# Performance work log

Measured on AMD Instinct MI355X. Metric: run time of the kernel, lower is better.

The kernel has to match this reference:

```python
import jax, jax.numpy as jnp
import numpy as np

HIDDEN = 1024
NUM_HEADS = 16
HEAD_DIM = HIDDEN // NUM_HEADS  # 64
B, LQ, LK = 2, 2048, 2048


def setup_inputs() -> dict:
    key = jax.random.key(0)
    ks = jax.random.split(key, 9)
    s = 1.0 / np.sqrt(HIDDEN)
    return {
        "hidden_states_query": jax.random.normal(ks[0], (B, LQ, HIDDEN), jnp.float32),
        "hidden_states_key": jax.random.normal(ks[1], (B, LK, HIDDEN), jnp.float32),
        "attention_mask": jnp.ones((B, LQ, LK), jnp.float32),
        "Wq": jax.random.normal(ks[2], (HIDDEN, HIDDEN), jnp.float32) * s,
        "bq": jax.random.normal(ks[3], (HIDDEN,), jnp.float32) * s,
        "Wk": jax.random.normal(ks[4], (HIDDEN, HIDDEN), jnp.float32) * s,
        "bk": jax.random.normal(ks[5], (HIDDEN,), jnp.float32) * s,
        "Wv": jax.random.normal(ks[6], (HIDDEN, HIDDEN), jnp.float32) * s,
        "bv": jax.random.normal(ks[7], (HIDDEN,), jnp.float32) * s,
    }


def _split_heads(x):
    # [B, L, H*D] -> [B, nH, L, D]
    b, l, _ = x.shape
    return x.reshape(b, l, NUM_HEADS, HEAD_DIM).transpose(0, 2, 1, 3)


def reference(hidden_states_query, hidden_states_key, attention_mask, Wq, bq, Wk, bk, Wv, bv):
    # nn.Linear applies x @ W.T + b; weights here stored as [out, in]
    q = _split_heads(hidden_states_query @ Wq.T + bq)
    k = _split_heads(hidden_states_key @ Wk.T + bk)
    v = _split_heads(hidden_states_key @ Wv.T + bv)
    scale = 1.0 / np.sqrt(HEAD_DIM)
    scores = jnp.einsum("bhqd,bhkd->bhqk", q * scale, k)  # [B, nH, Lq, Lk]
    # mask: 1 -> 0, 0 -> -10000, broadcast over heads
    scores = scores + ((1.0 - attention_mask) * -10000.0)[:, None, :, :]
    probs = jax.nn.softmax(scores, axis=-1)
    ctx = jnp.einsum("bhqk,bhkd->bhqd", probs, v)
    b, h, lq, d = ctx.shape
    return ctx.transpose(0, 2, 1, 3).reshape(b, lq, h * d)
```

## Files before the change

### kernel.cpp

```cpp
#include <hip/hip_runtime.h>
#include <hip/hip_bf16.h>

#define HID 1024
#define NH 16
#define HD 64
#define SEQ 2048
#define NB 2
#define NTOK (NB * SEQ)

typedef __attribute__((ext_vector_type(8))) short bf16x8;
typedef __attribute__((ext_vector_type(4))) float f32x4;

#define QSCALE 0.18033688011112042f
#define MASKSCALE 1.4426950408889634f

__device__ __forceinline__ unsigned short f2bf(float f) {
    unsigned u = __builtin_bit_cast(unsigned, f);
    u += 0x7FFFu + ((u >> 16) & 1u);
    return (unsigned short)(u >> 16);
}
__device__ __forceinline__ unsigned cvtpk(float a, float b) {
    unsigned r;
    asm("v_cvt_pk_bf16_f32 %0, %1, %2" : "=v"(r) : "v"(a), "v"(b));
    return r;
}
__device__ __forceinline__ void gload_lds16(const unsigned short* g, unsigned short* l) {
    __builtin_amdgcn_global_load_lds(
        (const __attribute__((address_space(1))) unsigned int*)g,
        (__attribute__((address_space(3))) unsigned int*)l, 16, 0, 0);
}

__global__ __launch_bounds__(256) void cvt_all(
    const float* __restrict__ xq, const float* __restrict__ xk,
    const float* __restrict__ Wq, const float* __restrict__ Wk, const float* __restrict__ Wv,
    const float* __restrict__ mask,
    unsigned short* __restrict__ dxq, unsigned short* __restrict__ dxk,
    unsigned short* __restrict__ dwq, unsigned short* __restrict__ dwk,
    unsigned short* __restrict__ dwv, int* __restrict__ flags) {
    const int id = blockIdx.x;
    if (id >= 11264) {
        const int lane = threadIdx.x & 63;
        int i = ((id - 11264) * 256 + threadIdx.x) * 4;
        float4 v = *(const float4*)(mask + i);
        bool ok = (v.x == 1.0f) && (v.y == 1.0f) && (v.z == 1.0f) && (v.w == 1.0f);
        unsigned long long bal = __ballot(ok);
        int g = lane >> 4;
        if ((lane & 15) == 0) {
            unsigned m16 = (unsigned)(bal >> (g * 16)) & 0xFFFFu;
            if (m16 != 0xFFFFu) {
                int b = i >> 22;
                int rem = i & 4194303;
                int q = rem >> 11, k = rem & 2047;
                atomicAnd(&flags[(b << 10) + ((q >> 6) << 5) + (k >> 6)], 0);
            }
        }
        return;
    }
    const float* src;
    unsigned short* dst;
    int base;
    float scale = 1.0f;
    if (id < 4096)       { src = xq; dst = dxq; base = 0; }
    else if (id < 8192)  { src = xk; dst = dxk; base = 4096; }
    else if (id < 9216)  { src = Wq; dst = dwq; base = 8192; scale = QSCALE; }
    else if (id < 10240) { src = Wk; dst = dwk; base = 9216; }
    else                 { src = Wv; dst = dwv; base = 10240; }
    int i = ((id - base) * 256 + threadIdx.x) * 4;
    float4 v = *(const float4*)(src + i);
    ushort4 o;
    o.x = f2bf(v.x * scale); o.y = f2bf(v.y * scale);
    o.z = f2bf(v.z * scale); o.w = f2bf(v.w * scale);
    *(ushort4*)(dst + i) = o;
}

__global__ __launch_bounds__(256) void proj_gemm(
    const unsigned short* __restrict__ xq, const unsigned short* __restrict__ xk,
    const unsigned short* __restrict__ wq, const unsigned short* __restrict__ wk,
    const unsigned short* __restrict__ wv,
    const float* __restrict__ bq, const float* __restrict__ bk, const float* __restrict__ bv,
    unsigned short* __restrict__ Qh, unsigned short* __restrict__ Kh,
    unsigned short* __restrict__ Vt) {
    __shared__ __align__(16) unsigned short As[128 * 32];
    __shared__ __align__(16) unsigned short Bs[128 * 32];

    const int z = blockIdx.z;
    const unsigned short *A, *B;
    const float* bias;
    float bsc;
    unsigned short* out;
    int mt, nt;
    bool tr;
    if (z == 0)      { A = xq; B = wq; bias = bq; bsc = QSCALE; out = Qh; tr = false; mt = blockIdx.x; nt = blockIdx.y; }
    else if (z == 1) { A = xk; B = wk; bias = bk; bsc = 1.0f;  out = Kh; tr = false; mt = blockIdx.x; nt = blockIdx.y; }
    else             { A = wv; B = xk; bias = bv; bsc = 1.0f;  out = Vt; tr = true;
                       mt = blockIdx.x & 7; nt = blockIdx.y * 4 + (blockIdx.x >> 3); }
    const int m0 = mt * 128, n0 = nt * 128;
    const int tid = threadIdx.x, wave = tid >> 6, lane = tid & 63;
    const int wr = (wave >> 1) * 64, wc = (wave & 1) * 64;
    const int frow = lane & 15, fk = (lane >> 4) * 8;
    const int srow = lane >> 2, skb = (lane & 3) * 8;

    f32x4 acc[4][4] = {};

    for (int k0 = 0; k0 < HID; k0 += 32) {
        __syncthreads();
#pragma unroll
        for (int t = 0; t < 2; ++t) {
            int c = t * 4 + wave;
            gload_lds16(A + (size_t)(m0 + c * 16 + srow) * HID + k0 + skb, &As[c * 512]);
            gload_lds16(B + (size_t)(n0 + c * 16 + srow) * HID + k0 + skb, &Bs[c * 512]);
        }
        __syncthreads();
        bf16x8 af[4], bfr[4];
#pragma unroll
        for (int i = 0; i < 4; ++i) af[i] = *(const bf16x8*)&As[(wr + i * 16 + frow) * 32 + fk];
#pragma unroll
        for (int j = 0; j < 4; ++j) bfr[j] = *(const bf16x8*)&Bs[(wc + j * 16 + frow) * 32 + fk];
#pragma unroll
        for (int i = 0; i < 4; ++i)
#pragma unroll
            for (int j = 0; j < 4; ++j)
                acc[i][j] = __builtin_amdgcn_mfma_f32_16x16x32_bf16(af[i], bfr[j], acc[i][j], 0, 0, 0);
    }

#pragma unroll
    for (int i = 0; i < 4; ++i)
#pragma unroll
        for (int j = 0; j < 4; ++j)
#pragma unroll
            for (int r = 0; r < 4; ++r) {
                int row = m0 + wr + i * 16 + (lane >> 4) * 4 + r;
                int col = n0 + wc + j * 16 + frow;
                float v = acc[i][j][r];
                if (!tr) {
                    v += bsc * bias[col];
                    int b = row >> 11, l = row & 2047, hh = col >> 6, d = col & 63;
                    out[(((size_t)(b * NH + hh)) * SEQ + l) * HD + d] = f2bf(v);
                } else {
                    v += bias[row];
                    int b = col >> 11, l = col & 2047, hh = row >> 6, d = row & 63;
                    out[(((size_t)(b * NH + hh)) * HD + d) * SEQ + l] = f2bf(v);
                }
            }
}

__global__ __launch_bounds__(256) void flash_attn(
    const unsigned short* __restrict__ Qh, const unsigned short* __restrict__ Kh,
    const unsigned short* __restrict__ Vt, const float* __restrict__ mask,
    const int* __restrict__ flags, float* __restrict__ out) {
    __shared__ __align__(16) unsigned short Ks[2][64 * 64];
    __shared__ __align__(16) unsigned short Vs[2][64 * 64];
    __shared__ __align__(16) unsigned short Ps[4][16 * 64];

    const int tid = threadIdx.x, wave = tid >> 6, lane = tid & 63;
    const int id = blockIdx.x;
    const int bh = (id & 7) * 4 + ((id >> 3) & 3);
    const int qi = id >> 5;
    const int b = bh >> 4, h = bh & 15;
    const size_t hoff = (size_t)bh * SEQ * HD;
    const int fr = lane & 15, hi = lane >> 4;
    const int f7 = fr & 7, swz3 = f7 << 3;
    const int qa = qi * 64 + wave * 16 + fr;

    bf16x8 qfa0 = *(const bf16x8*)&Qh[hoff + (size_t)qa * HD + hi * 8];
    bf16x8 qfa1 = *(const bf16x8*)&Qh[hoff + (size_t)qa * HD + 32 + hi * 8];

    const float* mrowA = mask + (size_t)b * SEQ * SEQ + (size_t)qa * SEQ;
    const int* frow = flags + (b << 10) + (qi << 5);
    int fv = frow[lane & 31];
    const unsigned long long bm = __ballot(fv != 0);

    const int srow = wave * 8 + (lane >> 3);
    const int sch = (lane & 7) ^ (srow & 7);
    const unsigned short* kbase = Kh + hoff + (size_t)srow * HD + (sch << 3);
    const unsigned short* vbase = Vt + hoff + (size_t)srow * SEQ + (sch << 3);

    f32x4 accA[4] = {};
    f32x4 laccA = {};
    const bf16x8 ones = {0x3F80, 0x3F80, 0x3F80, 0x3F80, 0x3F80, 0x3F80, 0x3F80, 0x3F80};

#define STAGE(bi, t)                                                              \
    do {                                                                          \
        gload_lds16(kbase + (size_t)(t) * 64 * HD, &Ks[bi][(wave * 8) * 64]);     \
        gload_lds16(kbase + (size_t)((t) * 64 + 32) * HD,                         \
                    &Ks[bi][(wave * 8 + 32) * 64]);                               \
        gload_lds16(vbase + (t) * 64, &Vs[bi][(wave * 8) * 64]);                  \
        gload_lds16(vbase + (size_t)32 * SEQ + (t) * 64,                          \
                    &Vs[bi][(wave * 8 + 32) * 64]);                               \
    } while (0)

    STAGE(0, 0);
    __syncthreads();
    int buf = 0;

    for (int t = 0; t < 32; ++t) {
        if (t < 31) STAGE(buf ^ 1, t + 1);
        const unsigned short* ks = Ks[buf];
        const unsigned short* vs = Vs[buf];

        f32x4 sA[4];
        __builtin_amdgcn_s_setprio(1);
#pragma unroll
        for (int sub = 0; sub < 4; ++sub) {
            const int rbase = (sub * 16 + fr) * 64;
            bf16x8 kf0 = *(const bf16x8*)&ks[rbase + ((hi << 3) ^ swz3)];
            bf16x8 kf1 = *(const bf16x8*)&ks[rbase + (((hi + 4) << 3) ^ swz3)];
            f32x4 z = {0.f, 0.f, 0.f, 0.f};
            z = __builtin_amdgcn_mfma_f32_16x16x32_bf16(kf0, qfa0, z, 0, 0, 0);
            z = __builtin_amdgcn_mfma_f32_16x16x32_bf16(kf1, qfa1, z, 0, 0, 0);
            sA[sub] = z;
        }
        __builtin_amdgcn_s_setprio(0);

        if (!((bm >> t) & 1)) {
            const int k0 = t * 64;
#pragma unroll
            for (int sub = 0; sub < 4; ++sub) {
                float4 ma = *(const float4*)&mrowA[k0 + sub * 16 + hi * 4];
                sA[sub][0] += (1.f - ma.x) * (-10000.f * MASKSCALE);
                sA[sub][1] += (1.f - ma.y) * (-10000.f * MASKSCALE);
                sA[sub][2] += (1.f - ma.z) * (-10000.f * MASKSCALE);
                sA[sub][3] += (1.f - ma.w) * (-10000.f * MASKSCALE);
            }
        }

#pragma unroll
        for (int sub = 0; sub < 4; ++sub)
#pragma unroll
            for (int r = 0; r < 4; ++r)
                sA[sub][r] = __builtin_amdgcn_exp2f(sA[sub][r]);

#pragma unroll
        for (int sub = 0; sub < 4; ++sub) {
            const int uoff = ((((sub << 1) + (hi >> 1)) ^ f7) << 3) + ((hi & 1) << 2);
            uint2 ua = {cvtpk(sA[sub][0], sA[sub][1]), cvtpk(sA[sub][2], sA[sub][3])};
            *(uint2*)&Ps[wave][fr * 64 + uoff] = ua;
        }

        bf16x8 pA0 = *(const bf16x8*)&Ps[wave][fr * 64 + ((hi ^ f7) << 3)];
        bf16x8 pA1 = *(const bf16x8*)&Ps[wave][fr * 64 + (((hi + 4) ^ f7) << 3)];

        __builtin_amdgcn_s_setprio(1);
        laccA = __builtin_amdgcn_mfma_f32_16x16x32_bf16(ones, pA0, laccA, 0, 0, 0);
        laccA = __builtin_amdgcn_mfma_f32_16x16x32_bf16(ones, pA1, laccA, 0, 0, 0);

#pragma unroll
        for (int sub = 0; sub < 4; ++sub) {
            const int rbase = (sub * 16 + fr) * 64;
            bf16x8 vf0 = *(const bf16x8*)&vs[rbase + ((hi << 3) ^ swz3)];
            bf16x8 vf1 = *(const bf16x8*)&vs[rbase + (((hi + 4) << 3) ^ swz3)];
            accA[sub] = __builtin_amdgcn_mfma_f32_16x16x32_bf16(vf0, pA0, accA[sub], 0, 0, 0);
            accA[sub] = __builtin_amdgcn_mfma_f32_16x16x32_bf16(vf1, pA1, accA[sub], 0, 0, 0);
        }
        __builtin_amdgcn_s_setprio(0);

        if (t < 31) {
            __syncthreads();
            buf ^= 1;
        }
    }

    float rA = 1.0f / laccA[0];
#pragma unroll
    for (int sub = 0; sub < 4; ++sub) {
        float4 oA = {accA[sub][0] * rA, accA[sub][1] * rA, accA[sub][2] * rA, accA[sub][3] * rA};
        *(float4*)&out[((size_t)b * SEQ + qa) * HID + h * HD + sub * 16 + hi * 4] = oA;
    }
#undef STAGE
}

extern "C" void kernel_launch(void* const* d_in, const int* in_sizes, int n_in,
                              void* d_out, int out_size, void* d_ws, size_t ws_size,
                              hipStream_t stream) {
    const float* xq = (const float*)d_in[0];
    const float* xk = (const float*)d_in[1];
    const float* mask = (const float*)d_in[2];
    const float* Wq = (const float*)d_in[3];
    const float* bq = (const float*)d_in[4];
    const float* Wk = (const float*)d_in[5];
    const float* bk = (const float*)d_in[6];
    const float* Wv = (const float*)d_in[7];
    const float* bv = (const float*)d_in[8];
    float* out = (float*)d_out;

    const size_t NX = (size_t)NTOK * HID;
    const size_t NW = (size_t)HID * HID;
    const size_t need = (5 * NX + 3 * NW) * sizeof(unsigned short) + 2048 * sizeof(int);
    if (ws_size < need) return;

    unsigned short* ws = (unsigned short*)d_ws;
    unsigned short* xq_b = ws;
    unsigned short* xk_b = xq_b + NX;
    unsigned short* wq_b = xk_b + NX;
    unsigned short* wk_b = wq_b + NW;
    unsigned short* wv_b = wk_b + NW;
    unsigned short* Qh = wv_b + NW;
    unsigned short* Kh = Qh + NX;
    unsigned short* Vt = Kh + NX;
    int* flags = (int*)(Vt + NX);

    hipMemsetAsync(flags, 0xFF, 2048 * sizeof(int), stream);
    cvt_all<<<19456, 256, 0, stream>>>(xq, xk, Wq, Wk, Wv, mask,
                                       xq_b, xk_b, wq_b, wk_b, wv_b, flags);
    proj_gemm<<<dim3(32, 8, 3), 256, 0, stream>>>(xq_b, xk_b, wq_b, wk_b, wv_b,
                                                  bq, bk, bv, Qh, Kh, Vt);
    flash_attn<<<1024, 256, 0, stream>>>(Qh, Kh, Vt, mask, flags, out);
}
```

Baseline: 121.8 us.

## Double-buffer projection GEMM loads and keep P fragments in registers via permuted V layout

The projection GEMM now double-buffers its LDS tiles: it prefetches the next K-slice while computing the current one and needs one barrier per iteration instead of two. The attention kernel drops the per-wave LDS round trip for the probability matrix. It packs the exp results directly into MFMA B-operand registers, and V^T columns are stored with a permuted sequence index so the register layout matches the reduction order. This removes LDS writes and reads plus latency in the inner attention loop, at the cost of doubled GEMM LDS use and a layout coupling that must match the K ordering exactly.

```diff
diff --git a/kernel.cpp b/kernel.cpp
--- a/kernel.cpp
+++ b/kernel.cpp
@@ -10,6 +10,7 @@
 
 typedef __attribute__((ext_vector_type(8))) short bf16x8;
 typedef __attribute__((ext_vector_type(4))) float f32x4;
+typedef __attribute__((ext_vector_type(4))) unsigned u32x4;
 
 #define QSCALE 0.18033688011112042f
 #define MASKSCALE 1.4426950408889634f
@@ -80,8 +81,8 @@
     const float* __restrict__ bq, const float* __restrict__ bk, const float* __restrict__ bv,
     unsigned short* __restrict__ Qh, unsigned short* __restrict__ Kh,
     unsigned short* __restrict__ Vt) {
-    __shared__ __align__(16) unsigned short As[128 * 32];
-    __shared__ __align__(16) unsigned short Bs[128 * 32];
+    __shared__ __align__(16) unsigned short As[2][128 * 32];
+    __shared__ __align__(16) unsigned short Bs[2][128 * 32];
 
     const int z = blockIdx.z;
     const unsigned short *A, *B;
@@ -100,27 +101,41 @@
     const int frow = lane & 15, fk = (lane >> 4) * 8;
     const int srow = lane >> 2, skb = (lane & 3) * 8;
 
+    const unsigned short* Ab = A + (size_t)(m0 + wave * 16 + srow) * HID + skb;
+    const unsigned short* Bb = B + (size_t)(n0 + wave * 16 + srow) * HID + skb;
+
     f32x4 acc[4][4] = {};
 
-    for (int k0 = 0; k0 < HID; k0 += 32) {
-        __syncthreads();
-#pragma unroll
-        for (int t = 0; t < 2; ++t) {
-            int c = t * 4 + wave;
-            gload_lds16(A + (size_t)(m0 + c * 16 + srow) * HID + k0 + skb, &As[c * 512]);
-            gload_lds16(B + (size_t)(n0 + c * 16 + srow) * HID + k0 + skb, &Bs[c * 512]);
-        }
-        __syncthreads();
+#define PSTAGE(bi, k0)                                                                 \
+    do {                                                                               \
+        gload_lds16(Ab + (k0), &As[bi][wave * 512]);                                   \
+        gload_lds16(Ab + (size_t)64 * HID + (k0), &As[bi][2048 + wave * 512]);         \
+        gload_lds16(Bb + (k0), &Bs[bi][wave * 512]);                                   \
+        gload_lds16(Bb + (size_t)64 * HID + (k0), &Bs[bi][2048 + wave * 512]);         \
+    } while (0)
+
+    PSTAGE(0, 0);
+    __syncthreads();
+    int buf = 0;
+
+    for (int it = 0; it < 32; ++it) {
+        if (it < 31) PSTAGE(buf ^ 1, (it + 1) * 32);
         bf16x8 af[4], bfr[4];
 #pragma unroll
-        for (int i = 0; i < 4; ++i) af[i] = *(const bf16x8*)&As[(wr + i * 16 + frow) * 32 + fk];
-#pragma unroll
-        for (int j = 0; j < 4; ++j) bfr[j] = *(const bf16x8*)&Bs[(wc + j * 16 + frow) * 32 + fk];
+        for (int i = 0; i < 4; ++i) af[i] = *(const bf16x8*)&As[buf][(wr + i * 16 + frow) * 32 + fk];
+#pragma unroll
+        for (int j = 0; j < 4; ++j) bfr[j] = *(const bf16x8*)&Bs[buf][(wc + j * 16 + frow) * 32 + fk];
+        __builtin_amdgcn_s_setprio(1);
 #pragma unroll
         for (int i = 0; i < 4; ++i)
 #pragma unroll
             for (int j = 0; j < 4; ++j)
                 acc[i][j] = __builtin_amdgcn_mfma_f32_16x16x32_bf16(af[i], bfr[j], acc[i][j], 0, 0, 0);
+        __builtin_amdgcn_s_setprio(0);
+        if (it < 31) {
+            __syncthreads();
+            buf ^= 1;
+        }
     }
 
 #pragma unroll
@@ -138,10 +153,12 @@
                     out[(((size_t)(b * NH + hh)) * SEQ + l) * HD + d] = f2bf(v);
                 } else {
                     v += bias[row];
-                    int b = col >> 11, l = col & 2047, hh = row >> 6, d = row & 63;
-                    out[(((size_t)(b * NH + hh)) * HD + d) * SEQ + l] = f2bf(v);
+                    int b = col >> 11, ll = col & 2047, hh = row >> 6, d = row & 63;
+                    int lp = (ll & ~0x1C) | ((ll & 0x0C) << 1) | ((ll & 0x10) >> 2);
+                    out[(((size_t)(b * NH + hh)) * HD + d) * SEQ + lp] = f2bf(v);
                 }
             }
+#undef PSTAGE
 }
 
 __global__ __launch_bounds__(256) void flash_attn(
@@ -150,7 +167,6 @@
     const int* __restrict__ flags, float* __restrict__ out) {
     __shared__ __align__(16) unsigned short Ks[2][64 * 64];
     __shared__ __align__(16) unsigned short Vs[2][64 * 64];
-    __shared__ __align__(16) unsigned short Ps[4][16 * 64];
 
     const int tid = threadIdx.x, wave = tid >> 6, lane = tid & 63;
     const int id = blockIdx.x;
@@ -230,15 +246,13 @@
             for (int r = 0; r < 4; ++r)
                 sA[sub][r] = __builtin_amdgcn_exp2f(sA[sub][r]);
 
-#pragma unroll
-        for (int sub = 0; sub < 4; ++sub) {
-            const int uoff = ((((sub << 1) + (hi >> 1)) ^ f7) << 3) + ((hi & 1) << 2);
-            uint2 ua = {cvtpk(sA[sub][0], sA[sub][1]), cvtpk(sA[sub][2], sA[sub][3])};
-            *(uint2*)&Ps[wave][fr * 64 + uoff] = ua;
-        }
-
-        bf16x8 pA0 = *(const bf16x8*)&Ps[wave][fr * 64 + ((hi ^ f7) << 3)];
-        bf16x8 pA1 = *(const bf16x8*)&Ps[wave][fr * 64 + (((hi + 4) ^ f7) << 3)];
+        u32x4 w0, w1;
+        w0[0] = cvtpk(sA[0][0], sA[0][1]); w0[1] = cvtpk(sA[0][2], sA[0][3]);
+        w0[2] = cvtpk(sA[1][0], sA[1][1]); w0[3] = cvtpk(sA[1][2], sA[1][3]);
+        w1[0] = cvtpk(sA[2][0], sA[2][1]); w1[1] = cvtpk(sA[2][2], sA[2][3]);
+        w1[2] = cvtpk(sA[3][0], sA[3][1]); w1[3] = cvtpk(sA[3][2], sA[3][3]);
+        bf16x8 pA0 = __builtin_bit_cast(bf16x8, w0);
+        bf16x8 pA1 = __builtin_bit_cast(bf16x8, w1);
 
         __builtin_amdgcn_s_setprio(1);
         laccA = __builtin_amdgcn_mfma_f32_16x16x32_bf16(ones, pA0, laccA, 0, 0, 0);
```

New measurement: 120.5 us. Within noise of the previous version (-1.1%).

## Triple-buffer projection GEMM with 256x128 tiles and keep P in registers

Applied to the files above, without the earlier changes.

The projection GEMM moves to 512-thread blocks with 256x128 tiles, a three-stage LDS ring with explicit vmcnt waits and a single barrier per k-step, and an XOR swizzle on the LDS layout. This is meant to overlap global loads with MFMA work and cut barrier and bank-conflict stalls. In flash attention, the P matrix is packed straight into MFMA operands instead of taking an LDS round trip, which is made correct by permuting the sequence index when V^T is written. The attention loop is also unrolled by two with fixed buffer pointers. The risks are lower GEMM occupancy from the larger LDS footprint and subtle layout coupling between the two kernels.

```diff
diff --git a/kernel.cpp b/kernel.cpp
--- a/kernel.cpp
+++ b/kernel.cpp
@@ -10,9 +10,12 @@
 
 typedef __attribute__((ext_vector_type(8))) short bf16x8;
 typedef __attribute__((ext_vector_type(4))) float f32x4;
+typedef __attribute__((ext_vector_type(4))) unsigned u32x4;
 
 #define QSCALE 0.18033688011112042f
 #define MASKSCALE 1.4426950408889634f
+
+#define MFMA16(a, b, c) __builtin_amdgcn_mfma_f32_16x16x32_bf16((a), (b), (c), 0, 0, 0)
 
 __device__ __forceinline__ unsigned short f2bf(float f) {
     unsigned u = __builtin_bit_cast(unsigned, f);
@@ -73,15 +76,15 @@
     *(ushort4*)(dst + i) = o;
 }
 
-__global__ __launch_bounds__(256) void proj_gemm(
+__global__ __launch_bounds__(512, 4) void proj_gemm(
     const unsigned short* __restrict__ xq, const unsigned short* __restrict__ xk,
     const unsigned short* __restrict__ wq, const unsigned short* __restrict__ wk,
     const unsigned short* __restrict__ wv,
     const float* __restrict__ bq, const float* __restrict__ bk, const float* __restrict__ bv,
     unsigned short* __restrict__ Qh, unsigned short* __restrict__ Kh,
     unsigned short* __restrict__ Vt) {
-    __shared__ __align__(16) unsigned short As[128 * 32];
-    __shared__ __align__(16) unsigned short Bs[128 * 32];
+    __shared__ __align__(16) unsigned short As[3][256 * 32];
+    __shared__ __align__(16) unsigned short Bs[3][128 * 32];
 
     const int z = blockIdx.z;
     const unsigned short *A, *B;
@@ -90,56 +93,87 @@
     unsigned short* out;
     int mt, nt;
     bool tr;
-    if (z == 0)      { A = xq; B = wq; bias = bq; bsc = QSCALE; out = Qh; tr = false; mt = blockIdx.x; nt = blockIdx.y; }
-    else if (z == 1) { A = xk; B = wk; bias = bk; bsc = 1.0f;  out = Kh; tr = false; mt = blockIdx.x; nt = blockIdx.y; }
+    if (z == 0)      { A = xq; B = wq; bias = bq; bsc = QSCALE; out = Qh; tr = false;
+                       mt = blockIdx.x & 15; nt = blockIdx.x >> 4; }
+    else if (z == 1) { A = xk; B = wk; bias = bk; bsc = 1.0f;  out = Kh; tr = false;
+                       mt = blockIdx.x & 15; nt = blockIdx.x >> 4; }
     else             { A = wv; B = xk; bias = bv; bsc = 1.0f;  out = Vt; tr = true;
-                       mt = blockIdx.x & 7; nt = blockIdx.y * 4 + (blockIdx.x >> 3); }
-    const int m0 = mt * 128, n0 = nt * 128;
+                       mt = blockIdx.x & 3; nt = blockIdx.x >> 2; }
+    const int m0 = mt * 256, n0 = nt * 128;
     const int tid = threadIdx.x, wave = tid >> 6, lane = tid & 63;
-    const int wr = (wave >> 1) * 64, wc = (wave & 1) * 64;
-    const int frow = lane & 15, fk = (lane >> 4) * 8;
-    const int srow = lane >> 2, skb = (lane & 3) * 8;
-
-    f32x4 acc[4][4] = {};
-
-    for (int k0 = 0; k0 < HID; k0 += 32) {
-        __syncthreads();
-#pragma unroll
-        for (int t = 0; t < 2; ++t) {
-            int c = t * 4 + wave;
-            gload_lds16(A + (size_t)(m0 + c * 16 + srow) * HID + k0 + skb, &As[c * 512]);
-            gload_lds16(B + (size_t)(n0 + c * 16 + srow) * HID + k0 + skb, &Bs[c * 512]);
+    const int wm = wave >> 2, wn = wave & 3;
+    const int fr = lane & 15, hi = lane >> 4;
+    const int fswz = (hi ^ ((fr >> 1) & 3)) << 3;
+
+    const int arow = wave * 16 + (lane >> 2);
+    const int aunit = (lane & 3) ^ ((lane >> 3) & 3);
+    const unsigned short* Asrc = A + (size_t)(m0 + arow) * HID + aunit * 8;
+    const unsigned short* Bsrc = B + (size_t)(n0 + arow) * HID + aunit * 8;
+
+    unsigned short *a0 = As[0], *a1 = As[1], *a2 = As[2];
+    unsigned short *b0 = Bs[0], *b1 = Bs[1], *b2 = Bs[2];
+
+    f32x4 acc[8][2] = {};
+
+#define PSTG(ap, bp, k0)                                                         \
+    do {                                                                         \
+        gload_lds16(Asrc + (k0), (ap) + wave * 512);                             \
+        gload_lds16(Asrc + (size_t)128 * HID + (k0), (ap) + 4096 + wave * 512);  \
+        gload_lds16(Bsrc + (k0), (bp) + wave * 512);                             \
+    } while (0)
+
+    PSTG(a0, b0, 0);
+    PSTG(a1, b1, 32);
+
+    for (int t = 0; t < 32; ++t) {
+        if (t < 31) asm volatile("s_waitcnt vmcnt(3)" ::: "memory");
+        else        asm volatile("s_waitcnt vmcnt(0)" ::: "memory");
+        __builtin_amdgcn_s_barrier();
+
+        bf16x8 bfr0 = *(const bf16x8*)&b0[(wn * 32 + fr) * 32 + fswz];
+        bf16x8 bfr1 = *(const bf16x8*)&b0[(wn * 32 + 16 + fr) * 32 + fswz];
+        if (t < 30) {
+            gload_lds16(Asrc + (t + 2) * 32, a2 + wave * 512);
+            gload_lds16(Asrc + (size_t)128 * HID + (t + 2) * 32, a2 + 4096 + wave * 512);
         }
-        __syncthreads();
-        bf16x8 af[4], bfr[4];
-#pragma unroll
-        for (int i = 0; i < 4; ++i) af[i] = *(const bf16x8*)&As[(wr + i * 16 + frow) * 32 + fk];
-#pragma unroll
-        for (int j = 0; j < 4; ++j) bfr[j] = *(const bf16x8*)&Bs[(wc + j * 16 + frow) * 32 + fk];
-#pragma unroll
-        for (int i = 0; i < 4; ++i)
-#pragma unroll
-            for (int j = 0; j < 4; ++j)
-                acc[i][j] = __builtin_amdgcn_mfma_f32_16x16x32_bf16(af[i], bfr[j], acc[i][j], 0, 0, 0);
+#pragma unroll
+        for (int mh = 0; mh < 2; ++mh) {
+            bf16x8 af[4];
+#pragma unroll
+            for (int i = 0; i < 4; ++i)
+                af[i] = *(const bf16x8*)&a0[(wm * 128 + mh * 64 + i * 16 + fr) * 32 + fswz];
+            if (mh == 0 && t < 30) gload_lds16(Bsrc + (t + 2) * 32, b2 + wave * 512);
+            __builtin_amdgcn_s_setprio(1);
+#pragma unroll
+            for (int i = 0; i < 4; ++i) {
+                acc[mh * 4 + i][0] = MFMA16(af[i], bfr0, acc[mh * 4 + i][0]);
+                acc[mh * 4 + i][1] = MFMA16(af[i], bfr1, acc[mh * 4 + i][1]);
+            }
+            __builtin_amdgcn_s_setprio(0);
+        }
+        unsigned short* ta = a0; a0 = a1; a1 = a2; a2 = ta;
+        unsigned short* tb = b0; b0 = b1; b1 = b2; b2 = tb;
     }
-
-#pragma unroll
-    for (int i = 0; i < 4; ++i)
-#pragma unroll
-        for (int j = 0; j < 4; ++j)
+#undef PSTG
+
+#pragma unroll
+    for (int ii = 0; ii < 8; ++ii)
+#pragma unroll
+        for (int j = 0; j < 2; ++j)
 #pragma unroll
             for (int r = 0; r < 4; ++r) {
-                int row = m0 + wr + i * 16 + (lane >> 4) * 4 + r;
-                int col = n0 + wc + j * 16 + frow;
-                float v = acc[i][j][r];
+                int row = m0 + wm * 128 + ii * 16 + hi * 4 + r;
+                int col = n0 + wn * 32 + j * 16 + fr;
+                float v = acc[ii][j][r];
                 if (!tr) {
                     v += bsc * bias[col];
                     int b = row >> 11, l = row & 2047, hh = col >> 6, d = col & 63;
                     out[(((size_t)(b * NH + hh)) * SEQ + l) * HD + d] = f2bf(v);
                 } else {
                     v += bias[row];
-                    int b = col >> 11, l = col & 2047, hh = row >> 6, d = row & 63;
-                    out[(((size_t)(b * NH + hh)) * HD + d) * SEQ + l] = f2bf(v);
+                    int b = col >> 11, ll = col & 2047, hh = row >> 6, d = row & 63;
+                    int lp = (ll & ~0x1C) | ((ll & 0x0C) << 1) | ((ll & 0x10) >> 2);
+                    out[(((size_t)(b * NH + hh)) * HD + d) * SEQ + lp] = f2bf(v);
                 }
             }
 }
@@ -150,7 +184,6 @@
     const int* __restrict__ flags, float* __restrict__ out) {
     __shared__ __align__(16) unsigned short Ks[2][64 * 64];
     __shared__ __align__(16) unsigned short Vs[2][64 * 64];
-    __shared__ __align__(16) unsigned short Ps[4][16 * 64];
 
     const int tid = threadIdx.x, wave = tid >> 6, lane = tid & 63;
     const int id = blockIdx.x;
@@ -172,93 +205,92 @@
 
     const int srow = wave * 8 + (lane >> 3);
     const int sch = (lane & 7) ^ (srow & 7);
-    const unsigned short* kbase = Kh + hoff + (size_t)srow * HD + (sch << 3);
-    const unsigned short* vbase = Vt + hoff + (size_t)srow * SEQ + (sch << 3);
+    const unsigned short* kp = Kh + hoff + (size_t)srow * HD + (sch << 3);
+    const unsigned short* vp = Vt + hoff + (size_t)srow * SEQ + (sch << 3);
 
     f32x4 accA[4] = {};
     f32x4 laccA = {};
     const bf16x8 ones = {0x3F80, 0x3F80, 0x3F80, 0x3F80, 0x3F80, 0x3F80, 0x3F80, 0x3F80};
 
-#define STAGE(bi, t)                                                              \
-    do {                                                                          \
-        gload_lds16(kbase + (size_t)(t) * 64 * HD, &Ks[bi][(wave * 8) * 64]);     \
-        gload_lds16(kbase + (size_t)((t) * 64 + 32) * HD,                         \
-                    &Ks[bi][(wave * 8 + 32) * 64]);                               \
-        gload_lds16(vbase + (t) * 64, &Vs[bi][(wave * 8) * 64]);                  \
-        gload_lds16(vbase + (size_t)32 * SEQ + (t) * 64,                          \
-                    &Vs[bi][(wave * 8 + 32) * 64]);                               \
+    unsigned short* const ks0 = &Ks[0][0];
+    unsigned short* const ks1 = &Ks[1][0];
+    unsigned short* const vs0 = &Vs[0][0];
+    unsigned short* const vs1 = &Vs[1][0];
+
+#define STG(ksd, vsd)                                                            \
+    do {                                                                         \
+        gload_lds16(kp, (ksd) + (wave * 8) * 64);                                \
+        gload_lds16(kp + (size_t)32 * HD, (ksd) + (wave * 8 + 32) * 64);         \
+        gload_lds16(vp, (vsd) + (wave * 8) * 64);                                \
+        gload_lds16(vp + (size_t)32 * SEQ, (vsd) + (wave * 8 + 32) * 64);        \
+        kp += 64 * HD; vp += 64;                                                 \
     } while (0)
 
-    STAGE(0, 0);
+#define FTILE(ks_, vs_, tt)                                                      \
+    do {                                                                         \
+        f32x4 sA[4];                                                             \
+        __builtin_amdgcn_s_setprio(1);                                           \
+        _Pragma("unroll")                                                        \
+        for (int sub = 0; sub < 4; ++sub) {                                      \
+            const int rbase = (sub * 16 + fr) * 64;                              \
+            bf16x8 kf0 = *(const bf16x8*)&(ks_)[rbase + ((hi << 3) ^ swz3)];     \
+            bf16x8 kf1 = *(const bf16x8*)&(ks_)[rbase + (((hi + 4) << 3) ^ swz3)]; \
+            f32x4 z = {0.f, 0.f, 0.f, 0.f};                                      \
+            z = MFMA16(kf0, qfa0, z);                                            \
+            z = MFMA16(kf1, qfa1, z);                                            \
+            sA[sub] = z;                                                         \
+        }                                                                        \
+        __builtin_amdgcn_s_setprio(0);                                           \
+        if (!((bm >> (tt)) & 1)) {                                               \
+            const int k0 = (tt) * 64;                                            \
+            _Pragma("unroll")                                                    \
+            for (int sub = 0; sub < 4; ++sub) {                                  \
+                float4 ma = *(const float4*)&mrowA[k0 + sub * 16 + hi * 4];      \
+                sA[sub][0] += (1.f - ma.x) * (-10000.f * MASKSCALE);             \
+                sA[sub][1] += (1.f - ma.y) * (-10000.f * MASKSCALE);             \
+                sA[sub][2] += (1.f - ma.z) * (-10000.f * MASKSCALE);             \
+                sA[sub][3] += (1.f - ma.w) * (-10000.f * MASKSCALE);             \
+            }                                                                    \
+        }                                                                        \
+        _Pragma("unroll")                                                        \
+        for (int sub = 0; sub < 4; ++sub)                                        \
+            _Pragma("unroll")                                                    \
+            for (int r = 0; r < 4; ++r)                                          \
+                sA[sub][r] = __builtin_amdgcn_exp2f(sA[sub][r]);                 \
+        u32x4 w0, w1;                                                            \
+        w0[0] = cvtpk(sA[0][0], sA[0][1]); w0[1] = cvtpk(sA[0][2], sA[0][3]);    \
+        w0[2] = cvtpk(sA[1][0], sA[1][1]); w0[3] = cvtpk(sA[1][2], sA[1][3]);    \
+        w1[0] = cvtpk(sA[2][0], sA[2][1]); w1[1] = cvtpk(sA[2][2], sA[2][3]);    \
+        w1[2] = cvtpk(sA[3][0], sA[3][1]); w1[3] = cvtpk(sA[3][2], sA[3][3]);    \
+        bf16x8 pA0 = __builtin_bit_cast(bf16x8, w0);                             \
+        bf16x8 pA1 = __builtin_bit_cast(bf16x8, w1);                             \
+        __builtin_amdgcn_s_setprio(1);                                           \
+        laccA = MFMA16(ones, pA0, laccA);                                        \
+        laccA = MFMA16(ones, pA1, laccA);                                        \
+        _Pragma("unroll")                                                        \
+        for (int sub = 0; sub < 4; ++sub) {                                      \
+            const int rbase = (sub * 16 + fr) * 64;                              \
+            bf16x8 vf0 = *(const bf16x8*)&(vs_)[rbase + ((hi << 3) ^ swz3)];     \
+            bf16x8 vf1 = *(const bf16x8*)&(vs_)[rbase + (((hi + 4) << 3) ^ swz3)]; \
+            accA[sub] = MFMA16(vf0, pA0, accA[sub]);                             \
+            accA[sub] = MFMA16(vf1, pA1, accA[sub]);                             \
+        }                                                                        \
+        __builtin_amdgcn_s_setprio(0);                                           \
+    } while (0)
+
+    STG(ks0, vs0);
     __syncthreads();
-    int buf = 0;
-
-    for (int t = 0; t < 32; ++t) {
-        if (t < 31) STAGE(buf ^ 1, t + 1);
-        const unsigned short* ks = Ks[buf];
-        const unsigned short* vs = Vs[buf];
-
-        f32x4 sA[4];
-        __builtin_amdgcn_s_setprio(1);
-#pragma unroll
-        for (int sub = 0; sub < 4; ++sub) {
-            const int rbase = (sub * 16 + fr) * 64;
-            bf16x8 kf0 = *(const bf16x8*)&ks[rbase + ((hi << 3) ^ swz3)];
-            bf16x8 kf1 = *(const bf16x8*)&ks[rbase + (((hi + 4) << 3) ^ swz3)];
-            f32x4 z = {0.f, 0.f, 0.f, 0.f};
-            z = __builtin_amdgcn_mfma_f32_16x16x32_bf16(kf0, qfa0, z, 0, 0, 0);
-            z = __builtin_amdgcn_mfma_f32_16x16x32_bf16(kf1, qfa1, z, 0, 0, 0);
-            sA[sub] = z;
-        }
-        __builtin_amdgcn_s_setprio(0);
-
-        if (!((bm >> t) & 1)) {
-            const int k0 = t * 64;
-#pragma unroll
-            for (int sub = 0; sub < 4; ++sub) {
-                float4 ma = *(const float4*)&mrowA[k0 + sub * 16 + hi * 4];
-                sA[sub][0] += (1.f - ma.x) * (-10000.f * MASKSCALE);
-                sA[sub][1] += (1.f - ma.y) * (-10000.f * MASKSCALE);
-                sA[sub][2] += (1.f - ma.z) * (-10000.f * MASKSCALE);
-                sA[sub][3] += (1.f - ma.w) * (-10000.f * MASKSCALE);
-            }
-        }
-
-#pragma unroll
-        for (int sub = 0; sub < 4; ++sub)
-#pragma unroll
-            for (int r = 0; r < 4; ++r)
-                sA[sub][r] = __builtin_amdgcn_exp2f(sA[sub][r]);
-
-#pragma unroll
-        for (int sub = 0; sub < 4; ++sub) {
-            const int uoff = ((((sub << 1) + (hi >> 1)) ^ f7) << 3) + ((hi & 1) << 2);
-            uint2 ua = {cvtpk(sA[sub][0], sA[sub][1]), cvtpk(sA[sub][2], sA[sub][3])};
-            *(uint2*)&Ps[wave][fr * 64 + uoff] = ua;
-        }
-
-        bf16x8 pA0 = *(const bf16x8*)&Ps[wave][fr * 64 + ((hi ^ f7) << 3)];
-        bf16x8 pA1 = *(const bf16x8*)&Ps[wave][fr * 64 + (((hi + 4) ^ f7) << 3)];
-
-        __builtin_amdgcn_s_setprio(1);
-        laccA = __builtin_amdgcn_mfma_f32_16x16x32_bf16(ones, pA0, laccA, 0, 0, 0);
-        laccA = __builtin_amdgcn_mfma_f32_16x16x32_bf16(ones, pA1, laccA, 0, 0, 0);
-
-#pragma unroll
-        for (int sub = 0; sub < 4; ++sub) {
-            const int rbase = (sub * 16 + fr) * 64;
-            bf16x8 vf0 = *(const bf16x8*)&vs[rbase + ((hi << 3) ^ swz3)];
-            bf16x8 vf1 = *(const bf16x8*)&vs[rbase + (((hi + 4) << 3) ^ swz3)];
-            accA[sub] = __builtin_amdgcn_mfma_f32_16x16x32_bf16(vf0, pA0, accA[sub], 0, 0, 0);
-            accA[sub] = __builtin_amdgcn_mfma_f32_16x16x32_bf16(vf1, pA1, accA[sub], 0, 0, 0);
-        }
-        __builtin_amdgcn_s_setprio(0);
-
-        if (t < 31) {
-            __syncthreads();
-            buf ^= 1;
-        }
+
+    for (int t2 = 0; t2 < 16; ++t2) {
+        STG(ks1, vs1);
+        FTILE(ks0, vs0, 2 * t2);
+        __syncthreads();
+        if (t2 < 15) STG(ks0, vs0);
+        FTILE(ks1, vs1, 2 * t2 + 1);
+        if (t2 < 15) __syncthreads();
     }
+#undef STG
+#undef FTILE
 
     float rA = 1.0f / laccA[0];
 #pragma unroll
@@ -266,7 +298,6 @@
         float4 oA = {accA[sub][0] * rA, accA[sub][1] * rA, accA[sub][2] * rA, accA[sub][3] * rA};
         *(float4*)&out[((size_t)b * SEQ + qa) * HID + h * HD + sub * 16 + hi * 4] = oA;
     }
-#undef STAGE
 }
 
 extern "C" void kernel_launch(void* const* d_in, const int* in_sizes, int n_in,
@@ -302,7 +333,7 @@
     hipMemsetAsync(flags, 0xFF, 2048 * sizeof(int), stream);
     cvt_all<<<19456, 256, 0, stream>>>(xq, xk, Wq, Wk, Wv, mask,
                                        xq_b, xk_b, wq_b, wk_b, wv_b, flags);
-    proj_gemm<<<dim3(32, 8, 3), 256, 0, stream>>>(xq_b, xk_b, wq_b, wk_b, wv_b,
-                                                  bq, bk, bv, Qh, Kh, Vt);
+    proj_gemm<<<dim3(128, 1, 3), 512, 0, stream>>>(xq_b, xk_b, wq_b, wk_b, wv_b,
+                                                   bq, bk, bv, Qh, Kh, Vt);
     flash_attn<<<1024, 256, 0, stream>>>(Qh, Kh, Vt, mask, flags, out);
 }
```

Result: faster. 112.2 us (-7.9%).
